# Kernel optimization log

Measured on AMD Instinct MI355X. Metric: run time of the kernel, lower is better.

## Reference

```python
import jax, jax.numpy as jnp
import numpy as np

B, D_IN, H, D_OUT = 1024, 512, 512, 512


def _act(v):
    # torch.relu(x) ** 2
    r = jnp.maximum(v, 0.0)
    return r * r


def setup_inputs() -> dict:
    key = jax.random.key(0)
    ks = jax.random.split(key, 8)
    x = jax.random.normal(ks[0], (B, D_IN), dtype=jnp.float32)
    # input_to_hidden: Linear(D_IN, H)
    W_in = jax.random.normal(ks[1], (D_IN, H), dtype=jnp.float32) / np.sqrt(D_IN)
    b_in = jax.random.normal(ks[2], (H,), dtype=jnp.float32) * 0.01
    # hidden_to_hidden[i]: Linear(1, H-i-1). Pack into padded arrays [H-1, H]
    # where row i, column j is the weight feeding output index j (valid only j > i).
    W_hh = jax.random.normal(ks[3], (H - 1, H), dtype=jnp.float32) * 0.02
    b_hh = jax.random.normal(ks[4], (H - 1, H), dtype=jnp.float32) * 0.01
    # hidden_to_output: Linear(H, D_OUT)
    W_out = jax.random.normal(ks[5], (H, D_OUT), dtype=jnp.float32) / np.sqrt(H)
    b_out = jax.random.normal(ks[6], (D_OUT,), dtype=jnp.float32) * 0.01
    return {"x": x, "W_in": W_in, "b_in": b_in, "W_hh": W_hh, "b_hh": b_hh,
            "W_out": W_out, "b_out": b_out}


def reference(x, W_in, b_in, W_hh, b_hh, W_out, b_out):
    h0 = _act(x @ W_in + b_in)  # [B, H]
    hid = h0.shape[1]
    col = jnp.arange(hid)

    def step(h, inp):
        i, w, b = inp  # w, b: [H] padded rows
        src = jnp.take(h, i, axis=1)  # [B], uses UPDATED h (strict sequential dep)
        contrib = _act(src[:, None] * w[None, :] + b[None, :])  # [B, H]
        mask = (col > i).astype(h.dtype)  # only columns i+1.. get updated
        return h + contrib * mask[None, :], None

    xs = (jnp.arange(hid - 1), W_hh, b_hh)
    h, _ = jax.lax.scan(step, h0, xs)
    return h @ W_out + b_out  # [B, D_OUT]
```

## Files before the change

### kernel.cpp

```cpp
#include <hip/hip_runtime.h>

#define B_SZ 1024
#define DIN 512
#define HH 512
#define DOUT 512

typedef short bf16x8 __attribute__((ext_vector_type(8)));
typedef float f32x4 __attribute__((ext_vector_type(4)));

__device__ __forceinline__ unsigned short f2bf(float f) {
    unsigned int u = __float_as_uint(f);
    u += 0x7FFFu + ((u >> 16) & 1u);
    return (unsigned short)(u >> 16);
}
__device__ __forceinline__ float bf2f(unsigned short s) {
    return __uint_as_float(((unsigned int)s) << 16);
}

__device__ __forceinline__ void conv_split_body(const float* __restrict__ src,
                                                uint4* __restrict__ dst, int t) {
    const int lane = t & 63;
    const int fb   = t >> 6;
    const int ks   = fb >> 6;
    const int mf   = fb & 63;
    const int row  = mf * 16 + (lane & 15);
    const int kb   = ks * 32 + ((lane >> 4) << 3);
    const int term = kb >> 9;
    const int c    = kb & 511;
    const float4 a0 = *(const float4*)&src[(size_t)row * 512 + c];
    const float4 a1 = *(const float4*)&src[(size_t)row * 512 + c + 4];
    const float av[8] = {a0.x, a0.y, a0.z, a0.w, a1.x, a1.y, a1.z, a1.w};
    unsigned short o[8];
    #pragma unroll
    for (int j = 0; j < 8; ++j) {
        unsigned short hi = f2bf(av[j]);
        o[j] = (term == 1) ? f2bf(av[j] - bf2f(hi)) : hi;
    }
    uint4 v;
    v.x = (unsigned int)o[0] | ((unsigned int)o[1] << 16);
    v.y = (unsigned int)o[2] | ((unsigned int)o[3] << 16);
    v.z = (unsigned int)o[4] | ((unsigned int)o[5] << 16);
    v.w = (unsigned int)o[6] | ((unsigned int)o[7] << 16);
    dst[t] = v;
}

__device__ __forceinline__ void convW_body(const float* __restrict__ W,
                                           uint4* __restrict__ dst, int t) {
    const int lane = t & 63;
    const int fb   = t >> 6;
    const int ks   = fb >> 5;
    const int nf   = fb & 31;
    const int col  = nf * 16 + (lane & 15);
    const int kb   = ks * 32 + ((lane >> 4) << 3);
    const int term = kb >> 9;
    const int c0   = kb & 511;
    unsigned short o[8];
    #pragma unroll
    for (int j = 0; j < 8; ++j) {
        const float f = W[(size_t)(c0 + j) * 512 + col];
        unsigned short hi = f2bf(f);
        o[j] = (term == 2) ? f2bf(f - bf2f(hi)) : hi;
    }
    uint4 v;
    v.x = (unsigned int)o[0] | ((unsigned int)o[1] << 16);
    v.y = (unsigned int)o[2] | ((unsigned int)o[3] << 16);
    v.z = (unsigned int)o[4] | ((unsigned int)o[5] << 16);
    v.w = (unsigned int)o[6] | ((unsigned int)o[7] << 16);
    dst[t] = v;
}

__global__ __launch_bounds__(256)
void prep_all(const float* __restrict__ W_hh, const float* __restrict__ b_hh,
              float2* __restrict__ wb,
              const float* __restrict__ x, uint4* __restrict__ Afr,
              const float* __restrict__ W_in, uint4* __restrict__ Bin,
              const float* __restrict__ W_out, uint4* __restrict__ Bout) {
    const int b = blockIdx.x;
    const int tid = threadIdx.x;
    if (b < 1022) {
        const int idx = b * 256 + tid;
        const int i = idx >> 9;
        const int j = idx & 511;
        float2 o;
        if (j > i) { o.x = W_hh[idx]; o.y = b_hh[idx]; }
        else       { o.x = 0.0f;      o.y = -1.0f;     }
        wb[idx] = o;
    } else if (b < 1790) {
        conv_split_body(x, Afr, (b - 1022) * 256 + tid);
    } else if (b < 2174) {
        convW_body(W_in, Bin, (b - 1790) * 256 + tid);
    } else {
        convW_body(W_out, Bout, (b - 2174) * 256 + tid);
    }
}

__global__ __launch_bounds__(256)
void conv_h(const float* __restrict__ h, uint4* __restrict__ Afr) {
    conv_split_body(h, Afr, blockIdx.x * 256 + threadIdx.x);
}

template <bool ACT>
__global__ __launch_bounds__(256)
void mfma_gemm(const uint4* __restrict__ Ag,
               const uint4* __restrict__ Bg,
               const float* __restrict__ bias,
               float* __restrict__ C) {
    __shared__ uint4 lds[2][768];
    const int tid  = threadIdx.x;
    const int lane = tid & 63;
    const int w    = tid >> 6;
    const int wr   = w & 1;
    const int wc   = w >> 1;
    const int mf0  = blockIdx.x * 4;
    const int nf0  = blockIdx.y * 2;

    const int a_mfs = (tid >> 6) & 3;
    const int b_ks  = tid >> 7;
    const int b_nfs = (tid >> 6) & 1;

    uint4 R0, R1, R2;
    auto stage = [&](int s) {
        const int ks0 = s * 2;
        R0 = Ag[(size_t)((ks0    ) * 64 + mf0 + a_mfs) * 64 + lane];
        R1 = Ag[(size_t)((ks0 + 1) * 64 + mf0 + a_mfs) * 64 + lane];
        R2 = Bg[(size_t)((ks0 + b_ks) * 32 + nf0 + b_nfs) * 64 + lane];
    };

    f32x4 acc0 = {0.f, 0.f, 0.f, 0.f};
    f32x4 acc1 = {0.f, 0.f, 0.f, 0.f};

    stage(0);
    lds[0][tid] = R0; lds[0][256 + tid] = R1; lds[0][512 + tid] = R2;
    stage(1);
    __syncthreads();

    for (int s = 0; s < 24; ++s) {
        const int cur = s & 1;
        if (s + 1 < 24) {
            const int nxt = cur ^ 1;
            lds[nxt][tid] = R0; lds[nxt][256 + tid] = R1; lds[nxt][512 + tid] = R2;
        }
        if (s + 2 < 24) stage(s + 2);
        __builtin_amdgcn_sched_barrier(0);

        bf16x8 aF[2][2], bF[2];
        #pragma unroll
        for (int ksL = 0; ksL < 2; ++ksL) {
            #pragma unroll
            for (int mfL = 0; mfL < 2; ++mfL)
                aF[ksL][mfL] = *(const bf16x8*)&lds[cur][ksL * 256 + (wr * 2 + mfL) * 64 + lane];
            bF[ksL] = *(const bf16x8*)&lds[cur][512 + (ksL * 2 + wc) * 64 + lane];
        }
        #pragma unroll
        for (int ksL = 0; ksL < 2; ++ksL) {
            acc0 = __builtin_amdgcn_mfma_f32_16x16x32_bf16(aF[ksL][0], bF[ksL], acc0, 0, 0, 0);
            acc1 = __builtin_amdgcn_mfma_f32_16x16x32_bf16(aF[ksL][1], bF[ksL], acc1, 0, 0, 0);
        }
        __syncthreads();
    }

    const int colg   = (nf0 + wc) * 16 + (lane & 15);
    const float bv   = bias[colg];
    const int rbase0 = (mf0 + wr * 2) * 16 + ((lane >> 4) << 2);
    #pragma unroll
    for (int r = 0; r < 4; ++r) {
        float v = acc0[r] + bv;
        if (ACT) { v = fmaxf(v, 0.f); v = v * v; }
        C[(size_t)(rbase0 + r) * 512 + colg] = v;
    }
    #pragma unroll
    for (int r = 0; r < 4; ++r) {
        float v = acc1[r] + bv;
        if (ACT) { v = fmaxf(v, 0.f); v = v * v; }
        C[(size_t)(rbase0 + 16 + r) * 512 + colg] = v;
    }
}

template <int C>
__device__ __forceinline__ void scan_chunk(const float2* __restrict__ wb,
                                           float2* __restrict__ smem,
                                           float hr[8], int lane) {
    constexpr int W2 = 64 * (8 - C);
    constexpr int T  = (C < 4) ? 8 : (C < 6 ? 16 : (C == 6 ? 32 : 64));
    constexpr int NTILES = 64 / T;
    constexpr int NLD = (T * W2) / 256;
    const int tid = threadIdx.x;

    float2 R[16];

    auto stage = [&](int i0) {
        #pragma unroll
        for (int q = 0; q < NLD; ++q) {
            const int e = tid + 256 * q;
            const int r = e / W2;
            const int col = e - r * W2;
            int row = i0 + r;
            if (row > 510) row = 510;
            R[q] = wb[(size_t)row * HH + 64 * C + col];
        }
    };

    stage(64 * C);
    for (int t = 0; t < NTILES; ++t) {
        __syncthreads();
        #pragma unroll
        for (int q = 0; q < NLD; ++q) smem[tid + 256 * q] = R[q];
        __syncthreads();
        if (t + 1 < NTILES) stage(64 * C + (t + 1) * T);
        __builtin_amdgcn_sched_barrier(0);

        #pragma unroll 4
        for (int r = 0; r < T; ++r) {
            const int ii = t * T + r;
            if (C == 7 && ii == 63) break;
            const float hi = __uint_as_float(
                __builtin_amdgcn_readlane(__float_as_uint(hr[C]), ii));
            #pragma unroll
            for (int k = C; k < 8; ++k) {
                const float2 wv = smem[r * W2 + lane + 64 * (k - C)];
                const float tv = fmaf(hi, wv.x, wv.y);
                const float rv = fmaxf(tv, 0.f);
                hr[k] = fmaf(rv, rv, hr[k]);
            }
        }
    }
}

__global__ __launch_bounds__(256)
void scan_kernel(const float2* __restrict__ wb, float* __restrict__ h) {
    __shared__ float2 smem[4096];
    const int lane = threadIdx.x & 63;
    const int wave = threadIdx.x >> 6;
    const int row  = blockIdx.x * 4 + wave;
    float* hrow = h + (size_t)row * HH;

    float hr[8];
    #pragma unroll
    for (int k = 0; k < 8; ++k) hr[k] = hrow[lane + 64 * k];

    scan_chunk<0>(wb, smem, hr, lane);
    scan_chunk<1>(wb, smem, hr, lane);
    scan_chunk<2>(wb, smem, hr, lane);
    scan_chunk<3>(wb, smem, hr, lane);
    scan_chunk<4>(wb, smem, hr, lane);
    scan_chunk<5>(wb, smem, hr, lane);
    scan_chunk<6>(wb, smem, hr, lane);
    scan_chunk<7>(wb, smem, hr, lane);

    #pragma unroll
    for (int k = 0; k < 8; ++k) hrow[lane + 64 * k] = hr[k];
}

extern "C" void kernel_launch(void* const* d_in, const int* in_sizes, int n_in,
                              void* d_out, int out_size, void* d_ws, size_t ws_size,
                              hipStream_t stream) {
    const float* x     = (const float*)d_in[0];
    const float* W_in  = (const float*)d_in[1];
    const float* b_in  = (const float*)d_in[2];
    const float* W_hh  = (const float*)d_in[3];
    const float* b_hh  = (const float*)d_in[4];
    const float* W_out = (const float*)d_in[5];
    const float* b_out = (const float*)d_in[6];
    float* out = (float*)d_out;

    char* ws = (char*)d_ws;
    float2* wb  = (float2*)ws;
    float*  h   = (float*)(ws + 0x200000u);
    uint4*  Afr = (uint4*)(ws + 0x400000u);
    uint4*  Bin = (uint4*)(ws + 0x700000u);
    uint4*  Bout= (uint4*)(ws + 0x880000u);

    prep_all<<<dim3(2558), dim3(256), 0, stream>>>(W_hh, b_hh, wb,
                                                   x, Afr, W_in, Bin, W_out, Bout);

    mfma_gemm<true><<<dim3(16, 16), dim3(256), 0, stream>>>(Afr, Bin, b_in, h);

    scan_kernel<<<dim3(256), dim3(256), 0, stream>>>(wb, h);

    conv_h<<<dim3(768), dim3(256), 0, stream>>>(h, Afr);

    mfma_gemm<false><<<dim3(16, 16), dim3(256), 0, stream>>>(Afr, Bout, b_out, out);
}
```

Measured before the change: 158.5 us.

## Stream scan weights directly from global memory into registers, dropping LDS staging

The scan kernel no longer stages weight/bias tiles into shared memory with block-wide barriers. Each wave now loads its own weight rows from global (L2-cached) memory into a register ring buffer, prefetching PF rows ahead of use. This removes __syncthreads and LDS traffic and lets the four waves in a block run independently. In exchange, every wave issues its own redundant global loads, and register pressure rises with the larger per-wave prefetch buffers.

```diff
diff --git a/kernel.cpp b/kernel.cpp
--- a/kernel.cpp
+++ b/kernel.cpp
@@ -178,57 +178,44 @@
 
 template <int C>
 __device__ __forceinline__ void scan_chunk(const float2* __restrict__ wb,
-                                           float2* __restrict__ smem,
                                            float hr[8], int lane) {
-    constexpr int W2 = 64 * (8 - C);
-    constexpr int T  = (C < 4) ? 8 : (C < 6 ? 16 : (C == 6 ? 32 : 64));
-    constexpr int NTILES = 64 / T;
-    constexpr int NLD = (T * W2) / 256;
-    const int tid = threadIdx.x;
-
-    float2 R[16];
-
-    auto stage = [&](int i0) {
-        #pragma unroll
-        for (int q = 0; q < NLD; ++q) {
-            const int e = tid + 256 * q;
-            const int r = e / W2;
-            const int col = e - r * W2;
-            int row = i0 + r;
-            if (row > 510) row = 510;
-            R[q] = wb[(size_t)row * HH + 64 * C + col];
-        }
-    };
-
-    stage(64 * C);
-    for (int t = 0; t < NTILES; ++t) {
-        __syncthreads();
-        #pragma unroll
-        for (int q = 0; q < NLD; ++q) smem[tid + 256 * q] = R[q];
-        __syncthreads();
-        if (t + 1 < NTILES) stage(64 * C + (t + 1) * T);
-        __builtin_amdgcn_sched_barrier(0);
-
-        #pragma unroll 4
-        for (int r = 0; r < T; ++r) {
-            const int ii = t * T + r;
-            if (C == 7 && ii == 63) break;
+    constexpr int NK = 8 - C;
+    constexpr int PF = (C < 4) ? 4 : (C < 6) ? 8 : 16;
+    constexpr int NT = 64 / PF;
+    const float2* base = wb + (size_t)(64 * C) * HH + 64 * C + lane;
+
+    float2 Wb[PF][NK];
+    #pragma unroll
+    for (int q = 0; q < PF; ++q)
+        #pragma unroll
+        for (int k = 0; k < NK; ++k)
+            Wb[q][k] = base[(size_t)q * HH + 64 * k];
+
+    for (int t = 0; t < NT; ++t) {
+        #pragma unroll
+        for (int q = 0; q < PF; ++q) {
+            const int s = t * PF + q;
             const float hi = __uint_as_float(
-                __builtin_amdgcn_readlane(__float_as_uint(hr[C]), ii));
-            #pragma unroll
-            for (int k = C; k < 8; ++k) {
-                const float2 wv = smem[r * W2 + lane + 64 * (k - C)];
-                const float tv = fmaf(hi, wv.x, wv.y);
-                const float rv = fmaxf(tv, 0.f);
-                hr[k] = fmaf(rv, rv, hr[k]);
+                __builtin_amdgcn_readlane(__float_as_uint(hr[C]), s));
+            if (C != 7 || s != 63) {
+                #pragma unroll
+                for (int k = 0; k < NK; ++k) {
+                    const float tv = fmaf(hi, Wb[q][k].x, Wb[q][k].y);
+                    const float rv = fmaxf(tv, 0.f);
+                    hr[C + k] = fmaf(rv, rv, hr[C + k]);
+                }
             }
+            if (t + 1 < NT) {
+                #pragma unroll
+                for (int k = 0; k < NK; ++k)
+                    Wb[q][k] = base[(size_t)(s + PF) * HH + 64 * k];
+            }
         }
     }
 }
 
 __global__ __launch_bounds__(256)
 void scan_kernel(const float2* __restrict__ wb, float* __restrict__ h) {
-    __shared__ float2 smem[4096];
     const int lane = threadIdx.x & 63;
     const int wave = threadIdx.x >> 6;
     const int row  = blockIdx.x * 4 + wave;
@@ -238,14 +225,14 @@
     #pragma unroll
     for (int k = 0; k < 8; ++k) hr[k] = hrow[lane + 64 * k];
 
-    scan_chunk<0>(wb, smem, hr, lane);
-    scan_chunk<1>(wb, smem, hr, lane);
-    scan_chunk<2>(wb, smem, hr, lane);
-    scan_chunk<3>(wb, smem, hr, lane);
-    scan_chunk<4>(wb, smem, hr, lane);
-    scan_chunk<5>(wb, smem, hr, lane);
-    scan_chunk<6>(wb, smem, hr, lane);
-    scan_chunk<7>(wb, smem, hr, lane);
+    scan_chunk<0>(wb, hr, lane);
+    scan_chunk<1>(wb, hr, lane);
+    scan_chunk<2>(wb, hr, lane);
+    scan_chunk<3>(wb, hr, lane);
+    scan_chunk<4>(wb, hr, lane);
+    scan_chunk<5>(wb, hr, lane);
+    scan_chunk<6>(wb, hr, lane);
+    scan_chunk<7>(wb, hr, lane);
 
     #pragma unroll
     for (int k = 0; k < 8; ++k) hrow[lane + 64 * k] = hr[k];
```

Result: no change. 157.4 us (-0.7%).
